# Performance work log

Measured on AMD Instinct MI355X. Metric: run time of the kernel, lower is better.

## Reference

```python
import jax, jax.numpy as jnp
import numpy as np

L = 8            # hash-grid levels
T = 1 << 19      # hashmap size per level (tcnn default log2_hashmap_size=19)
BASE = 16        # base_resolution
F = 2            # n_features_per_level
NEURONS = 128

_CORNERS = np.array([[(c >> 0) & 1, (c >> 1) & 1, (c >> 2) & 1] for c in range(8)], dtype=np.uint32)  # [8,3]
_PRIMES = np.array([1, 2654435761, 805459861], dtype=np.uint32)


def hash_grid_encode(x3, table):
    """Multi-resolution hash grid (instant-ngp style). x3:[N,3] in [0,1], table:[L,T,F]."""
    res = (BASE * (2.0 ** jnp.arange(L, dtype=jnp.float32)))        # per_level_scale = 2.0
    pos = x3[:, None, :] * res[None, :, None]                        # [N,L,3]
    p0 = jnp.floor(pos)
    frac = pos - p0                                                  # [N,L,3]
    p0i = p0.astype(jnp.uint32)
    corners = p0i[:, :, None, :] + jnp.asarray(_CORNERS)[None, None] # [N,L,8,3]
    pr = jnp.asarray(_PRIMES)
    h = (corners[..., 0] * pr[0]) ^ (corners[..., 1] * pr[1]) ^ (corners[..., 2] * pr[2])
    idx = (h & jnp.uint32(T - 1)).astype(jnp.int32)                  # [N,L,8]
    feats = table[jnp.arange(L)[None, :, None], idx]                 # [N,L,8,F]
    off = jnp.asarray(_CORNERS).astype(jnp.float32)                  # [8,3]
    w = jnp.prod(off[None, None] * frac[:, :, None, :] + (1.0 - off[None, None]) * (1.0 - frac[:, :, None, :]), axis=-1)  # [N,L,8]
    out = jnp.sum(feats * w[..., None], axis=2)                      # [N,L,F]
    return out.reshape(x3.shape[0], L * F)


def sh_encode_deg4(u3):
    """tcnn SphericalHarmonics degree 4: input in [0,1] mapped to [-1,1]. Returns [N,16]."""
    d = 2.0 * u3 - 1.0
    x, y, z = d[:, 0], d[:, 1], d[:, 2]
    x2, y2, z2 = x * x, y * y, z * z
    xy, yz, xz = x * y, y * z, x * z
    return jnp.stack([
        jnp.full_like(x, 0.28209479177387814),
        -0.48860251190291987 * y,
        0.48860251190291987 * z,
        -0.48860251190291987 * x,
        1.0925484305920792 * xy,
        -1.0925484305920792 * yz,
        0.94617469575755997 * z2 - 0.31539156525251999,
        -1.0925484305920792 * xz,
        0.54627421529603959 * (x2 - y2),
        0.59004358992664352 * y * (-3.0 * x2 + y2),
        2.8906114426405538 * xy * z,
        0.45704579946446572 * y * (1.0 - 5.0 * z2),
        0.3731763325901154 * z * (5.0 * z2 - 3.0),
        0.45704579946446572 * x * (1.0 - 5.0 * z2),
        1.445305721320277 * z * (x2 - y2),
        0.59004358992664352 * x * (-x2 + 3.0 * y2),
    ], axis=-1)


def setup_inputs() -> dict:
    key = jax.random.key(0)
    ks = jax.random.split(key, 8)
    N = 1048576
    x = jax.random.uniform(ks[0], (N, 6), dtype=jnp.float32)
    # hash table initialized small (tcnn-style uniform in [-1e-4, 1e-4])
    table = jax.random.uniform(ks[1], (L, T, F), minval=-1e-4, maxval=1e-4, dtype=jnp.float32)

    def lin(k, fan_in, fan_out):
        lim = float(1.0 / np.sqrt(fan_in))
        kw, kb = jax.random.split(k)
        W = jax.random.uniform(kw, (fan_out, fan_in), minval=-lim, maxval=lim, dtype=jnp.float32)
        b = jax.random.uniform(kb, (fan_out,), minval=-lim, maxval=lim, dtype=jnp.float32)
        return W, b

    enc_dim = L * F + 16  # 32
    W1, b1 = lin(ks[2], enc_dim, NEURONS)
    W2, b2 = lin(ks[3], NEURONS, NEURONS)
    W3, b3 = lin(ks[4], NEURONS, NEURONS)
    W4, b4 = lin(ks[5], NEURONS, 2)
    return dict(x=x, table=table, W1=W1, b1=b1, W2=W2, b2=b2, W3=W3, b3=b3, W4=W4, b4=b4)


def reference(x, table, W1, b1, W2, b2, W3, b3, W4, b4):
    enc = jnp.concatenate([hash_grid_encode(x[:, :3], table), sh_encode_deg4(x[:, 3:])], axis=-1)  # [N,32]
    h = jax.nn.relu(enc @ W1.T + b1)
    h = jax.nn.relu(h @ W2.T + b2)
    h = jax.nn.relu(h @ W3.T + b3)
    y = h @ W4.T + b4  # [N,2] -> torch.view_as_complex reinterprets as complex64 [N]
    return y
```

## Files before the change

### kernel.cpp

```cpp
#include <hip/hip_runtime.h>
#include <stdint.h>

#define TSIZE   (1u<<19)
#define P2c 2654435761u
#define P3c 805459861u

#define NTHR 512
#define BM 256

#define H_OFF   0u
#define W1_OFF  65536u
#define W2_OFF  73728u
#define W3_OFF  106496u
#define W4_OFF  139264u
#define B_OFF   143360u
#define LDS_BYTES 144960u

#define MW1   0u
#define MW2   8192u
#define MW3   40960u
#define MW4   73728u
#define MBIAS 77824u
#define MLP_LDS_BYTES 79872u

typedef _Float16 v8h __attribute__((ext_vector_type(8)));
typedef _Float16 v4h __attribute__((ext_vector_type(4)));
typedef float    v4f __attribute__((ext_vector_type(4)));

__device__ __forceinline__ uint32_t swz256(uint32_t row, uint32_t off){ return row*256u + (off ^ ((row&7u)<<4)); }
__device__ __forceinline__ uint32_t swz64 (uint32_t row, uint32_t off){ return row*64u  + (off ^ ((row&3u)<<4)); }

__device__ __forceinline__ uint32_t pkh(float a, float b){
  union { _Float16 h[2]; uint32_t u; } t;
  t.h[0] = (_Float16)a; t.h[1] = (_Float16)b; return t.u;
}
__device__ __forceinline__ v8h mk8(const uint32_t* w){
  union { uint32_t u[4]; v8h h; } t;
  t.u[0]=w[0]; t.u[1]=w[1]; t.u[2]=w[2]; t.u[3]=w[3]; return t.h;
}
__device__ __forceinline__ v4h mk4(uint32_t a, uint32_t b){
  union { uint32_t u[2]; v4h h; } t;
  t.u[0]=a; t.u[1]=b; return t.h;
}

__device__ __forceinline__ void sh16(float dx, float dy, float dz, float* s){
  float x2=dx*dx, y2=dy*dy, z2=dz*dz;
  float xy=dx*dy, yz=dy*dz, xz=dx*dz;
  s[0]=0.28209479177387814f;
  s[1]=-0.48860251190291987f*dy;
  s[2]= 0.48860251190291987f*dz;
  s[3]=-0.48860251190291987f*dx;
  s[4]= 1.0925484305920792f*xy;
  s[5]=-1.0925484305920792f*yz;
  s[6]= 0.94617469575756f*z2-0.31539156525252f;
  s[7]=-1.0925484305920792f*xz;
  s[8]= 0.5462742152960396f*(x2-y2);
  s[9]= 0.5900435899266435f*dy*(-3.f*x2+y2);
  s[10]=2.890611442640554f*xy*dz;
  s[11]=0.4570457994644657f*dy*(1.f-5.f*z2);
  s[12]=0.3731763325901154f*dz*(5.f*z2-3.f);
  s[13]=0.4570457994644657f*dx*(1.f-5.f*z2);
  s[14]=1.445305721320277f*dz*(x2-y2);
  s[15]=0.5900435899266435f*dx*(-x2+3.f*y2);
}

__global__ __launch_bounds__(256)
void cvt_table(const float* __restrict__ t, _Float16* __restrict__ o, int n4)
{
  int i = (int)(blockIdx.x*blockDim.x + threadIdx.x);
  int stride = (int)(gridDim.x*blockDim.x);
  for (; i < n4; i += stride){
    float4 v = ((const float4*)t)[i];
    v4h h; h[0]=(_Float16)v.x; h[1]=(_Float16)v.y; h[2]=(_Float16)v.z; h[3]=(_Float16)v.w;
    ((v4h*)o)[i] = h;
  }
}

__global__ __launch_bounds__(256)
void encode(const float* __restrict__ x, const _Float16* __restrict__ tb,
            uint32_t* __restrict__ planes, int N)
{
  const int lev = (int)(blockIdx.x & 7u);
  const int nch = (N + 511) >> 9;
  const uint32_t* lvl = (const uint32_t*)(tb + (size_t)lev*TSIZE*2u);
  const float res = (float)(16 << lev);
  const uint32_t m = TSIZE-1u;
  uint32_t* plane = planes + (size_t)lev*(size_t)N;
  for (int c = (int)(blockIdx.x >> 3); c < nch; c += (int)(gridDim.x >> 3)){
    int row0 = c*512 + (int)threadIdx.x;
    #pragma unroll
    for (int h=0; h<2; h++){
      int row = row0 + h*256;
      if (row < N){
        float px = x[row*6+0]*res, py = x[row*6+1]*res, pz = x[row*6+2]*res;
        float fx = floorf(px), fy = floorf(py), fz = floorf(pz);
        float rx = px-fx, ry = py-fy, rz = pz-fz;
        uint32_t ix=(uint32_t)fx, iy=(uint32_t)fy, iz=(uint32_t)fz;
        uint32_t hx0=ix,      hx1=ix+1u;
        uint32_t hy0=iy*P2c,  hy1=(iy+1u)*P2c;
        uint32_t hz0=iz*P3c,  hz1=(iz+1u)*P3c;
        uint32_t u0 = lvl[(hx0^hy0^hz0)&m];
        uint32_t u1 = lvl[(hx1^hy0^hz0)&m];
        uint32_t u2 = lvl[(hx0^hy1^hz0)&m];
        uint32_t u3 = lvl[(hx1^hy1^hz0)&m];
        uint32_t u4 = lvl[(hx0^hy0^hz1)&m];
        uint32_t u5 = lvl[(hx1^hy0^hz1)&m];
        uint32_t u6 = lvl[(hx0^hy1^hz1)&m];
        uint32_t u7 = lvl[(hx1^hy1^hz1)&m];
        float wx0=1.f-rx, wy0=1.f-ry, wz0=1.f-rz;
        float w0=wx0*wy0*wz0, w1=rx*wy0*wz0, w2=wx0*ry*wz0, w3=rx*ry*wz0;
        float w4=wx0*wy0*rz,  w5=rx*wy0*rz,  w6=wx0*ry*rz,  w7=rx*ry*rz;
        union { uint32_t u; _Float16 h[2]; } c0,c1,c2,c3,c4,c5,c6,c7;
        c0.u=u0; c1.u=u1; c2.u=u2; c3.u=u3; c4.u=u4; c5.u=u5; c6.u=u6; c7.u=u7;
        float s0 = (float)c0.h[0]*w0+(float)c1.h[0]*w1+(float)c2.h[0]*w2+(float)c3.h[0]*w3
                 + (float)c4.h[0]*w4+(float)c5.h[0]*w5+(float)c6.h[0]*w6+(float)c7.h[0]*w7;
        float s1 = (float)c0.h[1]*w0+(float)c1.h[1]*w1+(float)c2.h[1]*w2+(float)c3.h[1]*w3
                 + (float)c4.h[1]*w4+(float)c5.h[1]*w5+(float)c6.h[1]*w6+(float)c7.h[1]*w7;
        plane[row] = pkh(s0, s1);
      }
    }
  }
}

__global__ __launch_bounds__(512, 1)
void mlp_oneshot(const float* __restrict__ x, const uint32_t* __restrict__ planes,
                 const float* __restrict__ W1, const float* __restrict__ W2,
                 const float* __restrict__ W3, const float* __restrict__ W4,
                 const float* __restrict__ b1, const float* __restrict__ b2,
                 const float* __restrict__ b3, const float* __restrict__ b4,
                 float* __restrict__ out, int N)
{
  extern __shared__ char sm[];
  const int tid  = (int)threadIdx.x;
  const int lane = tid & 63;
  const int wave = tid >> 6;
  const int r = lane & 15;
  const int q = lane >> 4;

  for (int i = tid; i < 128*32; i += 512){
    int row = i >> 5, k = i & 31;
    uint32_t byte = (uint32_t)(k*2) ^ (uint32_t)((row&3)<<4);
    *(_Float16*)(sm + MW1 + (uint32_t)row*64u + byte) = (_Float16)W1[i];
  }
  for (int i = tid; i < 128*128; i += 512){
    int row = i >> 7, k = i & 127;
    uint32_t byte = (uint32_t)(k*2) ^ (uint32_t)((row&15)<<3);
    *(_Float16*)(sm + MW2 + (uint32_t)row*256u + byte) = (_Float16)W2[i];
    *(_Float16*)(sm + MW3 + (uint32_t)row*256u + byte) = (_Float16)W3[i];
  }
  for (int i = tid; i < 16*128; i += 512){
    int row = i >> 7, k = i & 127;
    uint32_t byte = (uint32_t)(k*2) ^ (uint32_t)((row&15)<<3);
    _Float16 v = (_Float16)0.f;
    if (i < 256) v = (_Float16)W4[i];
    *(_Float16*)(sm + MW4 + (uint32_t)row*256u + byte) = v;
  }
  {
    float* bl = (float*)(sm + MBIAS);
    for (int i = tid; i < 128; i += 512){ bl[i] = b1[i]; bl[128+i] = b2[i]; bl[256+i] = b3[i]; }
    if (tid < 2) bl[384+tid] = b4[tid];
  }
  __syncthreads();
  const float* bl = (const float*)(sm + MBIAS);

  const int R0 = (int)blockIdx.x*256 + wave*32;

  uint32_t b1w[2][4];
  #pragma unroll
  for (int rt=0; rt<2; rt++){
    int R  = R0 + rt*16 + r;
    int Rc = (R < N) ? R : 0;
    if (q < 2){
      #pragma unroll
      for (int i=0; i<4; i++)
        b1w[rt][i] = planes[(size_t)(q*4+i)*(size_t)N + (size_t)Rc];
    } else {
      float dx = 2.f*x[Rc*6+3]-1.f, dy = 2.f*x[Rc*6+4]-1.f, dz = 2.f*x[Rc*6+5]-1.f;
      float s[16]; sh16(dx, dy, dz, s);
      if (q == 2){
        b1w[rt][0]=pkh(s[0],s[1]);  b1w[rt][1]=pkh(s[2],s[3]);
        b1w[rt][2]=pkh(s[4],s[5]);  b1w[rt][3]=pkh(s[6],s[7]);
      } else {
        b1w[rt][0]=pkh(s[8],s[9]);   b1w[rt][1]=pkh(s[10],s[11]);
        b1w[rt][2]=pkh(s[12],s[13]); b1w[rt][3]=pkh(s[14],s[15]);
      }
    }
  }

  v4f acc[2][8];
  #pragma unroll
  for (int rt=0; rt<2; rt++)
    #pragma unroll
    for (int ct=0; ct<8; ct++){ v4f z={0.f,0.f,0.f,0.f}; acc[rt][ct]=z; }

  #pragma unroll
  for (int ct=0; ct<8; ct++){
    v8h a = *(const v8h*)(sm + MW1 + (uint32_t)(ct*16+r)*64u
                          + (uint32_t)((q*16) ^ ((r&3)<<4)));
    #pragma unroll
    for (int rt=0; rt<2; rt++)
      acc[rt][ct] = __builtin_amdgcn_mfma_f32_16x16x32_f16(a, mk8(b1w[rt]), acc[rt][ct], 0,0,0);
  }

  uint32_t bw[2][8][2];

  #define REPACK16(BL)                                                       \
    _Pragma("unroll")                                                        \
    for (int rt=0; rt<2; rt++){                                              \
      _Pragma("unroll")                                                      \
      for (int c=0; c<8; c++){                                               \
        float v0 = acc[rt][c][0] + BL[c*16 + q*4 + 0]; v0 = v0>0.f?v0:0.f;   \
        float v1 = acc[rt][c][1] + BL[c*16 + q*4 + 1]; v1 = v1>0.f?v1:0.f;   \
        float v2 = acc[rt][c][2] + BL[c*16 + q*4 + 2]; v2 = v2>0.f?v2:0.f;   \
        float v3 = acc[rt][c][3] + BL[c*16 + q*4 + 3]; v3 = v3>0.f?v3:0.f;   \
        bw[rt][c][0] = pkh(v0, v1);                                          \
        bw[rt][c][1] = pkh(v2, v3);                                          \
      }                                                                      \
    }

  #define HIDDEN16(WOFF)                                                     \
    _Pragma("unroll")                                                        \
    for (int rt=0; rt<2; rt++)                                               \
      _Pragma("unroll")                                                      \
      for (int ct=0; ct<8; ct++){ v4f z={0.f,0.f,0.f,0.f}; acc[rt][ct]=z; }  \
    _Pragma("unroll")                                                        \
    for (int c=0; c<8; c++){                                                 \
      _Pragma("unroll")                                                      \
      for (int ct=0; ct<8; ct++){                                            \
        v4h a = *(const v4h*)(sm + (WOFF) + (uint32_t)(ct*16+r)*256u         \
                              + (uint32_t)((c*32 + q*8) ^ (r<<3)));          \
        _Pragma("unroll")                                                    \
        for (int rt=0; rt<2; rt++)                                           \
          acc[rt][ct] = __builtin_amdgcn_mfma_f32_16x16x16f16(               \
              a, mk4(bw[rt][c][0], bw[rt][c][1]), acc[rt][ct], 0,0,0);       \
      }                                                                      \
    }

  REPACK16(bl)
  HIDDEN16(MW2)
  REPACK16((bl+128))
  HIDDEN16(MW3)
  REPACK16((bl+256))

  v4f a4[2];
  #pragma unroll
  for (int rt=0; rt<2; rt++){ v4f z={0.f,0.f,0.f,0.f}; a4[rt]=z; }
  #pragma unroll
  for (int c=0; c<8; c++){
    v4h a = *(const v4h*)(sm + MW4 + (uint32_t)r*256u
                          + (uint32_t)((c*32 + q*8) ^ (r<<3)));
    #pragma unroll
    for (int rt=0; rt<2; rt++)
      a4[rt] = __builtin_amdgcn_mfma_f32_16x16x16f16(
          a, mk4(bw[rt][c][0], bw[rt][c][1]), a4[rt], 0,0,0);
  }
  if (q == 0){
    float c0 = bl[384], c1 = bl[385];
    #pragma unroll
    for (int rt=0; rt<2; rt++){
      int R = R0 + rt*16 + r;
      if (R < N){
        float2 v; v.x = a4[rt][0] + c0; v.y = a4[rt][1] + c1;
        *(float2*)(out + (size_t)R*2) = v;
      }
    }
  }
  #undef REPACK16
  #undef HIDDEN16
}

template<int K, int O, int RTT, bool RELU>
__device__ __forceinline__ void mlp_layer(char* sm, uint32_t w_off, const float* bias, int wrow0, int lane)
{
  const int r = lane & 15;
  const int q = lane >> 4;
  v4f acc[RTT][O/16];
  #pragma unroll
  for (int rt=0;rt<RTT;rt++)
    #pragma unroll
    for (int ct=0;ct<O/16;ct++){ v4f z = {0.f,0.f,0.f,0.f}; acc[rt][ct] = z; }

  #pragma unroll
  for (int ks=0; ks<K/32; ks++){
    uint32_t abyte = (uint32_t)(ks*64 + q*16);
    v8h a[RTT];
    #pragma unroll
    for (int rt=0;rt<RTT;rt++)
      a[rt] = *(const v8h*)(sm + H_OFF + swz256((uint32_t)(wrow0 + rt*16 + r), abyte));
    #pragma unroll
    for (int ct=0; ct<O/16; ct++){
      uint32_t wrow = (uint32_t)(ct*16 + r);
      v8h b;
      if (K == 32) b = *(const v8h*)(sm + w_off + swz64 (wrow, abyte));
      else         b = *(const v8h*)(sm + w_off + swz256(wrow, abyte));
      #pragma unroll
      for (int rt=0;rt<RTT;rt++)
        acc[rt][ct] = __builtin_amdgcn_mfma_f32_16x16x32_f16(a[rt], b, acc[rt][ct], 0,0,0);
    }
  }
  #pragma unroll
  for (int rt=0;rt<RTT;rt++){
    #pragma unroll
    for (int ct=0; ct<O/16; ct++){
      float bv = bias[ct*16 + r];
      #pragma unroll
      for (int j=0;j<4;j++){
        float v = acc[rt][ct][j] + bv;
        if (RELU) v = v > 0.f ? v : 0.f;
        uint32_t row = (uint32_t)(wrow0 + rt*16 + q*4 + j);
        *(_Float16*)(sm + H_OFF + swz256(row, (uint32_t)((ct*16 + r)*2))) = (_Float16)v;
      }
    }
  }
}

__device__ __forceinline__ void sh_to_lds(char* sm, const float* __restrict__ x, int grow, uint32_t row)
{
  float dx = 2.f*x[grow*6+3]-1.f, dy = 2.f*x[grow*6+4]-1.f, dz = 2.f*x[grow*6+5]-1.f;
  float s[16]; sh16(dx,dy,dz,s);
  #pragma unroll
  for (int j=0;j<8;j++)
    *(uint32_t*)(sm + H_OFF + swz256(row, (uint32_t)(32 + 4*j))) = pkh(s[2*j], s[2*j+1]);
}

__global__ __launch_bounds__(NTHR, 2)
void ngp_fused(const float* __restrict__ x,
               const float* __restrict__ table,
               const float* __restrict__ W1, const float* __restrict__ b1,
               const float* __restrict__ W2, const float* __restrict__ b2,
               const float* __restrict__ W3, const float* __restrict__ b3,
               const float* __restrict__ W4, const float* __restrict__ b4,
               float* __restrict__ out, int N)
{
  extern __shared__ char sm[];
  const int tid  = (int)threadIdx.x;
  const int lane = tid & 63;
  const int wave = tid >> 6;

  for (int i = tid; i < 128*32; i += NTHR){
    uint32_t o = (uint32_t)(i >> 5), k = (uint32_t)(i & 31);
    *(_Float16*)(sm + W1_OFF + swz64(o, k*2u)) = (_Float16)W1[i];
  }
  for (int i = tid; i < 128*128; i += NTHR){
    uint32_t o = (uint32_t)(i >> 7), k = (uint32_t)(i & 127);
    *(_Float16*)(sm + W2_OFF + swz256(o, k*2u)) = (_Float16)W2[i];
    *(_Float16*)(sm + W3_OFF + swz256(o, k*2u)) = (_Float16)W3[i];
  }
  for (int i = tid; i < 2*128; i += NTHR){
    uint32_t o = (uint32_t)(i >> 7), k = (uint32_t)(i & 127);
    *(_Float16*)(sm + W4_OFF + swz256(o, k*2u)) = (_Float16)W4[i];
  }
  {
    float* bl = (float*)(sm + B_OFF);
    for (int i = tid; i < 128; i += NTHR){ bl[i] = b1[i]; bl[128+i] = b2[i]; bl[256+i] = b3[i]; }
    if (tid < 2) bl[384+tid] = b4[tid];
  }

  const int ntiles = (N + BM - 1) / BM;
  for (int tile = (int)blockIdx.x; tile < ntiles; tile += (int)gridDim.x){
    const int r0 = tile * BM;
    __syncthreads();

    #pragma unroll
    for (int t=0;t<4;t++){
      int task = t*NTHR + tid;
      int row  = task >> 3;
      int lev  = task & 7;
      int grow = r0 + row;
      if (grow < N){
        float px = x[grow*6+0], py = x[grow*6+1], pz = x[grow*6+2];
        float res = (float)(16 << lev);
        px *= res; py *= res; pz *= res;
        float fx = floorf(px), fy = floorf(py), fz = floorf(pz);
        float rx = px-fx, ry = py-fy, rz = pz-fz;
        uint32_t ix=(uint32_t)fx, iy=(uint32_t)fy, iz=(uint32_t)fz;
        uint32_t hx0=ix,      hx1=ix+1u;
        uint32_t hy0=iy*P2c,  hy1=(iy+1u)*P2c;
        uint32_t hz0=iz*P3c,  hz1=(iz+1u)*P3c;
        const float2* tbl = (const float2*)table + (size_t)lev*TSIZE;
        const uint32_t m = TSIZE-1u;
        float2 f0 = tbl[(hx0^hy0^hz0)&m];
        float2 f1 = tbl[(hx1^hy0^hz0)&m];
        float2 f2 = tbl[(hx0^hy1^hz0)&m];
        float2 f3 = tbl[(hx1^hy1^hz0)&m];
        float2 f4 = tbl[(hx0^hy0^hz1)&m];
        float2 f5 = tbl[(hx1^hy0^hz1)&m];
        float2 f6 = tbl[(hx0^hy1^hz1)&m];
        float2 f7 = tbl[(hx1^hy1^hz1)&m];
        float wx0=1.f-rx, wy0=1.f-ry, wz0=1.f-rz;
        float w0=wx0*wy0*wz0, w1=rx*wy0*wz0, w2=wx0*ry*wz0, w3=rx*ry*wz0;
        float w4=wx0*wy0*rz,  w5=rx*wy0*rz,  w6=wx0*ry*rz,  w7=rx*ry*rz;
        float s0 = f0.x*w0+f1.x*w1+f2.x*w2+f3.x*w3+f4.x*w4+f5.x*w5+f6.x*w6+f7.x*w7;
        float s1 = f0.y*w0+f1.y*w1+f2.y*w2+f3.y*w3+f4.y*w4+f5.y*w5+f6.y*w6+f7.y*w7;
        *(uint32_t*)(sm + H_OFF + swz256((uint32_t)row, (uint32_t)(lev*4))) = pkh(s0, s1);
      }
    }
    if (tid < BM){
      int row = tid, grow = r0 + row;
      if (grow < N) sh_to_lds(sm, x, grow, (uint32_t)row);
    }
    __syncthreads();

    const int wrow0 = wave * 32;
    const float* bl = (const float*)(sm + B_OFF);
    mlp_layer<32, 128, 2, true>(sm, W1_OFF, bl,       wrow0, lane);
    mlp_layer<128,128, 2, true>(sm, W2_OFF, bl + 128, wrow0, lane);
    mlp_layer<128,128, 2, true>(sm, W3_OFF, bl + 256, wrow0, lane);
    {
      const int r = lane & 15, q = lane >> 4;
      v4f acc0 = {0.f,0.f,0.f,0.f}, acc1 = {0.f,0.f,0.f,0.f};
      #pragma unroll
      for (int ks=0; ks<4; ks++){
        uint32_t abyte = (uint32_t)(ks*64 + q*16);
        v8h a0 = *(const v8h*)(sm + H_OFF + swz256((uint32_t)(wrow0 + r),      abyte));
        v8h a1 = *(const v8h*)(sm + H_OFF + swz256((uint32_t)(wrow0 + 16 + r), abyte));
        v8h b  = *(const v8h*)(sm + W4_OFF + swz256((uint32_t)r, abyte));
        acc0 = __builtin_amdgcn_mfma_f32_16x16x32_f16(a0, b, acc0, 0,0,0);
        acc1 = __builtin_amdgcn_mfma_f32_16x16x32_f16(a1, b, acc1, 0,0,0);
      }
      if (r < 2){
        float bv = bl[384 + r];
        #pragma unroll
        for (int j=0;j<4;j++){
          uint32_t row0 = (uint32_t)(wrow0 + q*4 + j);
          *(float*)(sm + H_OFF + swz256(row0,       (uint32_t)(r*4))) = acc0[j] + bv;
          *(float*)(sm + H_OFF + swz256(row0 + 16u, (uint32_t)(r*4))) = acc1[j] + bv;
        }
      }
    }
    __syncthreads();

    {
      int row = tid >> 1, col = tid & 1;
      int grow = r0 + row;
      if (grow < N){
        out[grow*2 + col] = *(const float*)(sm + H_OFF + swz256((uint32_t)row, (uint32_t)(col*4)));
      }
    }
  }
}

extern "C" void kernel_launch(void* const* d_in, const int* in_sizes, int n_in,
                              void* d_out, int out_size, void* d_ws, size_t ws_size,
                              hipStream_t stream)
{
  const float* x  = (const float*)d_in[0];
  const float* tb = (const float*)d_in[1];
  const float* W1 = (const float*)d_in[2];
  const float* b1 = (const float*)d_in[3];
  const float* W2 = (const float*)d_in[4];
  const float* b2 = (const float*)d_in[5];
  const float* W3 = (const float*)d_in[6];
  const float* b3 = (const float*)d_in[7];
  const float* W4 = (const float*)d_in[8];
  const float* b4 = (const float*)d_in[9];
  float* out = (float*)d_out;
  const int N = in_sizes[0] / 6;

  const size_t tbl16_bytes  = (size_t)8 * TSIZE * 2 * sizeof(_Float16);
  const size_t planes_bytes = (size_t)8 * (size_t)N * 4u;
  const size_t need = tbl16_bytes + planes_bytes;

  if (ws_size >= need){
    char* p = (char*)d_ws;
    _Float16* tbl16 = (_Float16*)p;                  p += tbl16_bytes;
    uint32_t* planes = (uint32_t*)p;

    (void)hipFuncSetAttribute((const void*)mlp_oneshot,
                              hipFuncAttributeMaxDynamicSharedMemorySize, (int)MLP_LDS_BYTES);

    cvt_table<<<2048, 256, 0, stream>>>(tb, tbl16, (int)(8u*TSIZE*2u/4u));
    encode<<<4096, 256, 0, stream>>>(x, tbl16, planes, N);

    const int ntiles = (N + 255) / 256;
    mlp_oneshot<<<ntiles, 512, MLP_LDS_BYTES, stream>>>(x, planes, W1, W2, W3, W4,
                                                        b1, b2, b3, b4, out, N);
  } else {
    (void)hipFuncSetAttribute((const void*)ngp_fused,
                              hipFuncAttributeMaxDynamicSharedMemorySize, (int)LDS_BYTES);
    const int ntiles = (N + BM - 1) / BM;
    const int grid = ntiles < 1024 ? ntiles : 1024;
    ngp_fused<<<grid, NTHR, LDS_BYTES, stream>>>(x, tb, W1, b1, W2, b2, W3, b3, W4, b4, out, N);
  }
}
```

Before: 294.6 us.

## Precompute swizzled fp16 weight image and packed xyz buffer before encode/MLP

Adds a small kernel that converts the MLP weights and biases once into the swizzled fp16 LDS image, so each MLP block copies it with float4 loads instead of converting per block. Also adds a prep pass that packs the xyz coordinates into float4 so the eight per-level encode passes read 16-byte aligned rows instead of strided 6-float rows. Both add extra launches and workspace traffic, and the xyz path only runs when the workspace is large enough.

```diff
diff --git a/kernel.cpp b/kernel.cpp
--- a/kernel.cpp
+++ b/kernel.cpp
@@ -22,6 +22,7 @@
 #define MW4   73728u
 #define MBIAS 77824u
 #define MLP_LDS_BYTES 79872u
+#define WIMG_BYTES 81920u
 
 typedef _Float16 v8h __attribute__((ext_vector_type(8)));
 typedef _Float16 v4h __attribute__((ext_vector_type(4)));
@@ -77,8 +78,80 @@
 }
 
 __global__ __launch_bounds__(256)
-void encode(const float* __restrict__ x, const _Float16* __restrict__ tb,
-            uint32_t* __restrict__ planes, int N)
+void cvt_wimg(const float* __restrict__ W1, const float* __restrict__ W2,
+              const float* __restrict__ W3, const float* __restrict__ W4,
+              const float* __restrict__ b1, const float* __restrict__ b2,
+              const float* __restrict__ b3, const float* __restrict__ b4,
+              char* __restrict__ img)
+{
+  int i = (int)(blockIdx.x*256 + threadIdx.x);
+  if (i < 128*32){
+    int row = i >> 5, k = i & 31;
+    uint32_t byte = (uint32_t)(k*2) ^ (uint32_t)((row&3)<<4);
+    *(_Float16*)(img + MW1 + (uint32_t)row*64u + byte) = (_Float16)W1[i];
+  }
+  if (i < 128*128){
+    int row = i >> 7, k = i & 127;
+    uint32_t byte = (uint32_t)(k*2) ^ (uint32_t)((row&15)<<3);
+    *(_Float16*)(img + MW2 + (uint32_t)row*256u + byte) = (_Float16)W2[i];
+    *(_Float16*)(img + MW3 + (uint32_t)row*256u + byte) = (_Float16)W3[i];
+  }
+  if (i < 16*128){
+    int row = i >> 7, k = i & 127;
+    uint32_t byte = (uint32_t)(k*2) ^ (uint32_t)((row&15)<<3);
+    _Float16 v = (i < 256) ? (_Float16)W4[i] : (_Float16)0.f;
+    *(_Float16*)(img + MW4 + (uint32_t)row*256u + byte) = v;
+  }
+  if (i < 128){
+    float* bl = (float*)(img + MBIAS);
+    bl[i] = b1[i]; bl[128+i] = b2[i]; bl[256+i] = b3[i];
+    if (i < 2) bl[384+i] = b4[i];
+  }
+}
+
+__global__ __launch_bounds__(256)
+void prep_xyz(const float* __restrict__ x, float4* __restrict__ xyz, int N)
+{
+  int i = (int)(blockIdx.x*256 + threadIdx.x);
+  int stride = (int)(gridDim.x*256);
+  for (; i < N; i += stride){
+    float4 v; v.x = x[i*6+0]; v.y = x[i*6+1]; v.z = x[i*6+2]; v.w = 0.f;
+    xyz[i] = v;
+  }
+}
+
+__device__ __forceinline__ uint32_t enc_row(const uint32_t* __restrict__ lvl,
+                                            float px, float py, float pz, uint32_t m)
+{
+  float fx = floorf(px), fy = floorf(py), fz = floorf(pz);
+  float rx = px-fx, ry = py-fy, rz = pz-fz;
+  uint32_t ix=(uint32_t)fx, iy=(uint32_t)fy, iz=(uint32_t)fz;
+  uint32_t hx0=ix,      hx1=ix+1u;
+  uint32_t hy0=iy*P2c,  hy1=(iy+1u)*P2c;
+  uint32_t hz0=iz*P3c,  hz1=(iz+1u)*P3c;
+  uint32_t u0 = lvl[(hx0^hy0^hz0)&m];
+  uint32_t u1 = lvl[(hx1^hy0^hz0)&m];
+  uint32_t u2 = lvl[(hx0^hy1^hz0)&m];
+  uint32_t u3 = lvl[(hx1^hy1^hz0)&m];
+  uint32_t u4 = lvl[(hx0^hy0^hz1)&m];
+  uint32_t u5 = lvl[(hx1^hy0^hz1)&m];
+  uint32_t u6 = lvl[(hx0^hy1^hz1)&m];
+  uint32_t u7 = lvl[(hx1^hy1^hz1)&m];
+  float wx0=1.f-rx, wy0=1.f-ry, wz0=1.f-rz;
+  float w0=wx0*wy0*wz0, w1=rx*wy0*wz0, w2=wx0*ry*wz0, w3=rx*ry*wz0;
+  float w4=wx0*wy0*rz,  w5=rx*wy0*rz,  w6=wx0*ry*rz,  w7=rx*ry*rz;
+  union { uint32_t u; _Float16 h[2]; } c0,c1,c2,c3,c4,c5,c6,c7;
+  c0.u=u0; c1.u=u1; c2.u=u2; c3.u=u3; c4.u=u4; c5.u=u5; c6.u=u6; c7.u=u7;
+  float s0 = (float)c0.h[0]*w0+(float)c1.h[0]*w1+(float)c2.h[0]*w2+(float)c3.h[0]*w3
+           + (float)c4.h[0]*w4+(float)c5.h[0]*w5+(float)c6.h[0]*w6+(float)c7.h[0]*w7;
+  float s1 = (float)c0.h[1]*w0+(float)c1.h[1]*w1+(float)c2.h[1]*w2+(float)c3.h[1]*w3
+           + (float)c4.h[1]*w4+(float)c5.h[1]*w5+(float)c6.h[1]*w6+(float)c7.h[1]*w7;
+  return pkh(s0, s1);
+}
+
+__global__ __launch_bounds__(256)
+void encode4(const float4* __restrict__ xyz, const _Float16* __restrict__ tb,
+             uint32_t* __restrict__ planes, int N)
 {
   const int lev = (int)(blockIdx.x & 7u);
   const int nch = (N + 511) >> 9;
@@ -92,31 +165,30 @@
     for (int h=0; h<2; h++){
       int row = row0 + h*256;
       if (row < N){
-        float px = x[row*6+0]*res, py = x[row*6+1]*res, pz = x[row*6+2]*res;
-        float fx = floorf(px), fy = floorf(py), fz = floorf(pz);
-        float rx = px-fx, ry = py-fy, rz = pz-fz;
-        uint32_t ix=(uint32_t)fx, iy=(uint32_t)fy, iz=(uint32_t)fz;
-        uint32_t hx0=ix,      hx1=ix+1u;
-        uint32_t hy0=iy*P2c,  hy1=(iy+1u)*P2c;
-        uint32_t hz0=iz*P3c,  hz1=(iz+1u)*P3c;
-        uint32_t u0 = lvl[(hx0^hy0^hz0)&m];
-        uint32_t u1 = lvl[(hx1^hy0^hz0)&m];
-        uint32_t u2 = lvl[(hx0^hy1^hz0)&m];
-        uint32_t u3 = lvl[(hx1^hy1^hz0)&m];
-        uint32_t u4 = lvl[(hx0^hy0^hz1)&m];
-        uint32_t u5 = lvl[(hx1^hy0^hz1)&m];
-        uint32_t u6 = lvl[(hx0^hy1^hz1)&m];
-        uint32_t u7 = lvl[(hx1^hy1^hz1)&m];
-        float wx0=1.f-rx, wy0=1.f-ry, wz0=1.f-rz;
-        float w0=wx0*wy0*wz0, w1=rx*wy0*wz0, w2=wx0*ry*wz0, w3=rx*ry*wz0;
-        float w4=wx0*wy0*rz,  w5=rx*wy0*rz,  w6=wx0*ry*rz,  w7=rx*ry*rz;
-        union { uint32_t u; _Float16 h[2]; } c0,c1,c2,c3,c4,c5,c6,c7;
-        c0.u=u0; c1.u=u1; c2.u=u2; c3.u=u3; c4.u=u4; c5.u=u5; c6.u=u6; c7.u=u7;
-        float s0 = (float)c0.h[0]*w0+(float)c1.h[0]*w1+(float)c2.h[0]*w2+(float)c3.h[0]*w3
-                 + (float)c4.h[0]*w4+(float)c5.h[0]*w5+(float)c6.h[0]*w6+(float)c7.h[0]*w7;
-        float s1 = (float)c0.h[1]*w0+(float)c1.h[1]*w1+(float)c2.h[1]*w2+(float)c3.h[1]*w3
-                 + (float)c4.h[1]*w4+(float)c5.h[1]*w5+(float)c6.h[1]*w6+(float)c7.h[1]*w7;
-        plane[row] = pkh(s0, s1);
+        float4 p = xyz[row];
+        plane[row] = enc_row(lvl, p.x*res, p.y*res, p.z*res, m);
+      }
+    }
+  }
+}
+
+__global__ __launch_bounds__(256)
+void encode(const float* __restrict__ x, const _Float16* __restrict__ tb,
+            uint32_t* __restrict__ planes, int N)
+{
+  const int lev = (int)(blockIdx.x & 7u);
+  const int nch = (N + 511) >> 9;
+  const uint32_t* lvl = (const uint32_t*)(tb + (size_t)lev*TSIZE*2u);
+  const float res = (float)(16 << lev);
+  const uint32_t m = TSIZE-1u;
+  uint32_t* plane = planes + (size_t)lev*(size_t)N;
+  for (int c = (int)(blockIdx.x >> 3); c < nch; c += (int)(gridDim.x >> 3)){
+    int row0 = c*512 + (int)threadIdx.x;
+    #pragma unroll
+    for (int h=0; h<2; h++){
+      int row = row0 + h*256;
+      if (row < N){
+        plane[row] = enc_row(lvl, x[row*6+0]*res, x[row*6+1]*res, x[row*6+2]*res, m);
       }
     }
   }
@@ -124,10 +196,7 @@
 
 __global__ __launch_bounds__(512, 1)
 void mlp_oneshot(const float* __restrict__ x, const uint32_t* __restrict__ planes,
-                 const float* __restrict__ W1, const float* __restrict__ W2,
-                 const float* __restrict__ W3, const float* __restrict__ W4,
-                 const float* __restrict__ b1, const float* __restrict__ b2,
-                 const float* __restrict__ b3, const float* __restrict__ b4,
+                 const float4* __restrict__ wimg,
                  float* __restrict__ out, int N)
 {
   extern __shared__ char sm[];
@@ -137,28 +206,9 @@
   const int r = lane & 15;
   const int q = lane >> 4;
 
-  for (int i = tid; i < 128*32; i += 512){
-    int row = i >> 5, k = i & 31;
-    uint32_t byte = (uint32_t)(k*2) ^ (uint32_t)((row&3)<<4);
-    *(_Float16*)(sm + MW1 + (uint32_t)row*64u + byte) = (_Float16)W1[i];
-  }
-  for (int i = tid; i < 128*128; i += 512){
-    int row = i >> 7, k = i & 127;
-    uint32_t byte = (uint32_t)(k*2) ^ (uint32_t)((row&15)<<3);
-    *(_Float16*)(sm + MW2 + (uint32_t)row*256u + byte) = (_Float16)W2[i];
-    *(_Float16*)(sm + MW3 + (uint32_t)row*256u + byte) = (_Float16)W3[i];
-  }
-  for (int i = tid; i < 16*128; i += 512){
-    int row = i >> 7, k = i & 127;
-    uint32_t byte = (uint32_t)(k*2) ^ (uint32_t)((row&15)<<3);
-    _Float16 v = (_Float16)0.f;
-    if (i < 256) v = (_Float16)W4[i];
-    *(_Float16*)(sm + MW4 + (uint32_t)row*256u + byte) = v;
-  }
   {
-    float* bl = (float*)(sm + MBIAS);
-    for (int i = tid; i < 128; i += 512){ bl[i] = b1[i]; bl[128+i] = b2[i]; bl[256+i] = b3[i]; }
-    if (tid < 2) bl[384+tid] = b4[tid];
+    float4* l = (float4*)sm;
+    for (int j = tid; j < (int)(MLP_LDS_BYTES/16); j += 512) l[j] = wimg[j];
   }
   __syncthreads();
   const float* bl = (const float*)(sm + MBIAS);
@@ -368,17 +418,16 @@
       int lev  = task & 7;
       int grow = r0 + row;
       if (grow < N){
-        float px = x[grow*6+0], py = x[grow*6+1], pz = x[grow*6+2];
+        const float2* tbl = (const float2*)table + (size_t)lev*TSIZE;
+        const uint32_t m = TSIZE-1u;
         float res = (float)(16 << lev);
-        px *= res; py *= res; pz *= res;
+        float px = x[grow*6+0]*res, py = x[grow*6+1]*res, pz = x[grow*6+2]*res;
         float fx = floorf(px), fy = floorf(py), fz = floorf(pz);
         float rx = px-fx, ry = py-fy, rz = pz-fz;
         uint32_t ix=(uint32_t)fx, iy=(uint32_t)fy, iz=(uint32_t)fz;
         uint32_t hx0=ix,      hx1=ix+1u;
         uint32_t hy0=iy*P2c,  hy1=(iy+1u)*P2c;
         uint32_t hz0=iz*P3c,  hz1=(iz+1u)*P3c;
-        const float2* tbl = (const float2*)table + (size_t)lev*TSIZE;
-        const uint32_t m = TSIZE-1u;
         float2 f0 = tbl[(hx0^hy0^hz0)&m];
         float2 f1 = tbl[(hx1^hy0^hz0)&m];
         float2 f2 = tbl[(hx0^hy1^hz0)&m];
@@ -459,22 +508,32 @@
 
   const size_t tbl16_bytes  = (size_t)8 * TSIZE * 2 * sizeof(_Float16);
   const size_t planes_bytes = (size_t)8 * (size_t)N * 4u;
-  const size_t need = tbl16_bytes + planes_bytes;
-
-  if (ws_size >= need){
+  const size_t xyz_bytes    = (size_t)N * 16u;
+  const size_t need_mid  = tbl16_bytes + planes_bytes + WIMG_BYTES;
+  const size_t need_full = need_mid + xyz_bytes;
+
+  if (ws_size >= need_mid){
     char* p = (char*)d_ws;
     _Float16* tbl16 = (_Float16*)p;                  p += tbl16_bytes;
-    uint32_t* planes = (uint32_t*)p;
+    uint32_t* planes = (uint32_t*)p;                 p += planes_bytes;
+    char*     wimg  = p;                             p += WIMG_BYTES;
+    float4*   xyz   = (float4*)p;
 
     (void)hipFuncSetAttribute((const void*)mlp_oneshot,
                               hipFuncAttributeMaxDynamicSharedMemorySize, (int)MLP_LDS_BYTES);
 
     cvt_table<<<2048, 256, 0, stream>>>(tb, tbl16, (int)(8u*TSIZE*2u/4u));
-    encode<<<4096, 256, 0, stream>>>(x, tbl16, planes, N);
+    cvt_wimg<<<64, 256, 0, stream>>>(W1, W2, W3, W4, b1, b2, b3, b4, wimg);
+
+    if (ws_size >= need_full){
+      prep_xyz<<<2048, 256, 0, stream>>>(x, xyz, N);
+      encode4<<<4096, 256, 0, stream>>>(xyz, tbl16, planes, N);
+    } else {
+      encode<<<4096, 256, 0, stream>>>(x, tbl16, planes, N);
+    }
 
     const int ntiles = (N + 255) / 256;
-    mlp_oneshot<<<ntiles, 512, MLP_LDS_BYTES, stream>>>(x, planes, W1, W2, W3, W4,
-                                                        b1, b2, b3, b4, out, N);
+    mlp_oneshot<<<ntiles, 512, MLP_LDS_BYTES, stream>>>(x, planes, (const float4*)wimg, out, N);
   } else {
     (void)hipFuncSetAttribute((const void*)ngp_fused,
                               hipFuncAttributeMaxDynamicSharedMemorySize, (int)LDS_BYTES);
```

Result: faster. 280.8 us (-4.7%).
